# Performance work log

Hardware: AMD Instinct MI355X
Metric: run time of the kernel (lower is better)

The kernel has to match this reference:

```python
import jax, jax.numpy as jnp
import numpy as np
from jax import lax

B, W, M = 4, 20, 512
RNN_HID = 64
N_HIDDEN = RNN_HID          # bi = False
HALF = N_HIDDEN // 2
K = 10
LONG_K = W // 2             # conv_long kernel
LONG_OUT = W - 2 * (LONG_K - 1)   # = 2
N_SPATIAL = 10


def setup_inputs() -> dict:
    key = jax.random.key(0)
    ks = jax.random.split(key, 24)
    g = lambda i, shape, s=0.05: jax.random.normal(ks[i], shape, jnp.float32) * s
    return {
        "x": jax.random.normal(ks[0], (B, W, M), jnp.float32),
        # vanilla RNN (tanh), 1 layer, input_size=1
        "W_ih": g(1, (RNN_HID, 1), 0.2), "W_hh": g(2, (RNN_HID, RNN_HID), 0.1),
        "b_ih": g(3, (RNN_HID,)), "b_hh": g(4, (RNN_HID,)),
        # attention adjacency params
        "W1": g(5, (HALF, N_HIDDEN), 0.1), "b1": g(6, (HALF,)),
        "W2": g(7, (HALF, N_HIDDEN), 0.1),
        "V": g(8, (HALF,), 0.1), "bv": g(9, (1,)),
        "Wb": g(10, (M, M), 0.05), "wb": g(11, (1,)),
        # conv / conv_long
        "conv_w": g(12, (K, 1, W), 0.1), "conv_b": g(13, (K,)),
        "convl_w": g(14, (K, 1, LONG_K), 0.1), "convl_b": g(15, (K,)),
        # graph conv layers: adj @ (x @ W) + b
        "gc1_w": g(16, ((1 + LONG_OUT) * K, N_HIDDEN), 0.1), "gc1_b": g(17, (N_HIDDEN,)),
        "gc2_w": g(18, (N_HIDDEN, N_SPATIAL), 0.1), "gc2_b": g(19, (N_SPATIAL,)),
        # output head
        "out_w": g(20, (1, N_HIDDEN + N_SPATIAL), 0.1), "out_b": g(21, (1,)),
        # fixed geographic adjacency (data.adj)
        "adj": jax.random.uniform(ks[22], (M, M), dtype=jnp.float32),
    }


def _conv1d(x, w, b, dilation=1):
    # x: (N, Cin, W), w: (Cout, Cin, K) -> (N, Cout, Wout), VALID padding
    y = lax.conv_general_dilated(x, w, (1,), 'VALID', rhs_dilation=(dilation,),
                                 dimension_numbers=('NCH', 'OIH', 'NCH'))
    return y + b[None, :, None]


def reference(x, W_ih, W_hh, b_ih, b_hh, W1, b1, W2, V, bv, Wb, wb,
              conv_w, conv_b, convl_w, convl_b, gc1_w, gc1_b, gc2_w, gc2_b,
              out_w, out_b, adj):
    b, w, m = x.shape
    # ---- RNN encode each node's scalar series: (b*m, w, 1) -> last hidden ----
    xr = jnp.transpose(x, (0, 2, 1)).reshape(b * m, w)          # (bm, w)
    inp = xr[..., None] @ W_ih.T + b_ih                         # (bm, w, H)

    def step(h, u):
        return jnp.tanh(u + h @ W_hh.T + b_hh), None

    h0 = jnp.zeros((b * m, RNN_HID), x.dtype)
    h_last, _ = lax.scan(step, h0, jnp.swapaxes(inp, 0, 1))     # (bm, H)
    last_hid = h_last.reshape(b, m, N_HIDDEN)
    out_temporal = last_hid

    # ---- pairwise bilinear attention adjacency (broadcast instead of repeat) ----
    p = last_hid @ W1.T                                         # (b, m, H/2)
    q = last_hid @ W2.T                                         # (b, m, H/2)
    e = jax.nn.elu(p[:, :, None, :] + q[:, None, :, :] + b1)    # (b, m, m, H/2)
    a_mx = e @ V + bv[0]                                        # (b, m, m)
    # F.normalize(p=2, dim=1)
    nrm = jnp.maximum(jnp.sqrt(jnp.sum(a_mx * a_mx, axis=1, keepdims=True)), 1e-12)
    a_mx = a_mx / nrm
    c = jax.nn.sigmoid(a_mx @ Wb + wb[0])                       # (b, m, m)
    A = adj[None] * c + a_mx * (1.0 - c)

    # ---- per-node convs, batched over all b*m series (no Python loop) ----
    h_tmp = xr[:, None, :]                                      # (bm, 1, w)
    r = _conv1d(h_tmp, conv_w, conv_b)                          # (bm, k, 1)
    r_long = _conv1d(h_tmp, convl_w, convl_b, dilation=2)       # (bm, k, long_out)
    r_l = jnp.concatenate([r, r_long], axis=-1).reshape(b, m, -1)  # (b, m, (1+lo)*k)
    r_l = jax.nn.relu(r_l)

    # ---- graph convolutions: adj @ (x @ W) + b ----
    xg = jax.nn.relu(A @ (r_l @ gc1_w) + gc1_b)                 # (b, m, H)
    out_spatial = jax.nn.relu(A @ (xg @ gc2_w) + gc2_b)         # (b, m, 10)

    out = jnp.concatenate([out_spatial, out_temporal], axis=-1)
    return (out @ out_w.T + out_b)[..., 0]                      # (b, m)
```

## Files before the change

### kernel.cpp

```cpp
#include <hip/hip_runtime.h>
#include <hip/hip_bf16.h>
#include <cstdint>
#include <cstddef>

#define OFF_P     0
#define OFF_QB    65536
#define OFF_TDOT  131072
#define OFF_COLSQ 133120
#define OFF_ZT    135168
#define OFF_AMXB  155648
#define OFF_ABF   679936
#define OFF_G1T   1204224
#define OFF_WBT   1269760

typedef __attribute__((ext_vector_type(8))) short short8;
typedef __attribute__((ext_vector_type(8))) unsigned short ushort8;
typedef __attribute__((ext_vector_type(4))) float f32x4;

__device__ inline unsigned short f2bf(float f) {
    unsigned u = __builtin_bit_cast(unsigned, f);
    unsigned r = u + 0x7FFFu + ((u >> 16) & 1u);
    return (unsigned short)(r >> 16);
}
__device__ inline unsigned short f2bf_fast(float f) {
    unsigned u = __builtin_bit_cast(unsigned, f);
    return (unsigned short)((u + 0x8000u) >> 16);
}
__device__ inline float bf2f(unsigned short s) {
    unsigned u = ((unsigned)s) << 16;
    return __builtin_bit_cast(float, u);
}
__device__ inline float tanh_fast(float x) {
    return 1.f - 2.f/(__expf(2.f*x) + 1.f);
}

__global__ __launch_bounds__(256) void k1_rnn(
    const float* __restrict__ x, const float* __restrict__ W_ih,
    const float* __restrict__ W_hh, const float* __restrict__ b_ih,
    const float* __restrict__ b_hh, const float* __restrict__ W1,
    const float* __restrict__ b1, const float* __restrict__ W2,
    const float* __restrict__ conv_w, const float* __restrict__ conv_b,
    const float* __restrict__ convl_w, const float* __restrict__ convl_b,
    const float* __restrict__ gc1_w, const float* __restrict__ out_w,
    const float* __restrict__ out_b, const float* __restrict__ Wb,
    float* __restrict__ p_out, float* __restrict__ qb_out,
    unsigned short* __restrict__ G1T, float* __restrict__ tdot,
    float* __restrict__ colsq, unsigned short* __restrict__ WbT)
{
    __shared__ float h_sh[4][64];
    __shared__ float xt_sh[4][20];
    __shared__ float rl_sh[4][30];
    __shared__ float tile[64][68];
    int tid = threadIdx.x;

    if (blockIdx.x >= 512) {
        int tt = blockIdx.x - 512;
        int k0 = (tt >> 3) * 64, j0 = (tt & 7) * 64;
        #pragma unroll
        for (int q = 0; q < 4; ++q) {
            int kr = (tid>>4) + 16*q;
            int jc = (tid&15)*4;
            *(float4*)&tile[kr][jc] = *(const float4*)(Wb + (size_t)(k0+kr)*512 + j0 + jc);
        }
        __syncthreads();
        int jl = tid>>2, kc = (tid&3)*16;
        int j = j0 + jl;
        ushort8 v0, v1;
        #pragma unroll
        for (int kk = 0; kk < 8; ++kk) v0[kk] = f2bf(tile[kc+kk][jl]);
        #pragma unroll
        for (int kk = 0; kk < 8; ++kk) v1[kk] = f2bf(tile[kc+8+kk][jl]);
        unsigned short* dst = WbT + (size_t)j*512 + k0 + kc;
        *(ushort8*)dst = v0;
        *(ushort8*)(dst+8) = v1;
        return;
    }

    int w = tid >> 6, lane = tid & 63;
    int s = blockIdx.x * 4 + w;
    int b = s >> 9, m = s & 511;

    if (blockIdx.x < 8) colsq[blockIdx.x * 256 + tid] = 0.f;

    if (lane < 20) xt_sh[w][lane] = x[(b*20 + lane)*512 + m];

    float wrow[64];
    const float* wr = W_hh + lane*64;
    #pragma unroll
    for (int k4 = 0; k4 < 16; ++k4) {
        float4 v = reinterpret_cast<const float4*>(wr)[k4];
        wrow[4*k4+0]=v.x; wrow[4*k4+1]=v.y; wrow[4*k4+2]=v.z; wrow[4*k4+3]=v.w;
    }
    float wih = W_ih[lane], bih = b_ih[lane], bhh = b_hh[lane];
    h_sh[w][lane] = 0.f;
    float h = 0.f;

    if (lane < 10) {
        float acc = conv_b[lane];
        #pragma unroll
        for (int t = 0; t < 20; ++t) acc += conv_w[lane*20+t]*xt_sh[w][t];
        rl_sh[w][3*lane] = fmaxf(acc, 0.f);
    } else if (lane < 30) {
        int idx = lane-10, j = idx>>1, oo = idx&1;
        float acc = convl_b[j];
        #pragma unroll
        for (int t = 0; t < 10; ++t) acc += convl_w[j*10+t]*xt_sh[w][oo+2*t];
        rl_sh[w][3*j+1+oo] = fmaxf(acc, 0.f);
    }

    for (int t = 0; t < 20; ++t) {
        float a0=0.f, a1=0.f, a2=0.f, a3=0.f;
        #pragma unroll
        for (int k = 0; k < 64; k += 4) {
            a0 += wrow[k+0]*h_sh[w][k+0];
            a1 += wrow[k+1]*h_sh[w][k+1];
            a2 += wrow[k+2]*h_sh[w][k+2];
            a3 += wrow[k+3]*h_sh[w][k+3];
        }
        float acc = xt_sh[w][t]*wih + bih + bhh + ((a0+a1)+(a2+a3));
        h = tanh_fast(acc);
        h_sh[w][lane] = h;
    }

    float td = h * out_w[10 + lane];
    #pragma unroll
    for (int off = 32; off; off >>= 1) td += __shfl_down(td, off);
    if (lane == 0) tdot[s] = td + out_b[0];

    if (lane < 32) {
        const float* w1r = W1 + lane*64;
        float acc = 0.f;
        #pragma unroll
        for (int k = 0; k < 64; ++k) acc += w1r[k]*h_sh[w][k];
        p_out[s*32 + lane] = acc;
    } else {
        int i = lane - 32;
        const float* w2r = W2 + i*64;
        float acc = 0.f;
        #pragma unroll
        for (int k = 0; k < 64; ++k) acc += w2r[k]*h_sh[w][k];
        qb_out[s*32 + i] = acc + b1[i];
    }

    float g = 0.f;
    #pragma unroll
    for (int t = 0; t < 30; ++t) g += rl_sh[w][t]*gc1_w[t*64 + lane];
    G1T[((size_t)(b*64 + lane))*512 + m] = f2bf(g);
}

__global__ __launch_bounds__(256) void k2_amx(
    const float* __restrict__ p, const float* __restrict__ qb,
    const float* __restrict__ V, const float* __restrict__ bv,
    unsigned short* __restrict__ amxB, float* __restrict__ colsq)
{
    __shared__ float p_sh[32*36], q_sh[32*36], v_sh[32], sq_sh[32*17];
    int t = threadIdx.x;
    int b = blockIdx.z, i0 = blockIdx.y*32, j0 = blockIdx.x*32;
    {
        int r = t >> 3, c4 = (t & 7)*4;
        *(float4*)&p_sh[r*36 + c4] = *(const float4*)(p  + (size_t)(b*512 + i0 + r)*32 + c4);
        *(float4*)&q_sh[r*36 + c4] = *(const float4*)(qb + (size_t)(b*512 + j0 + r)*32 + c4);
    }
    if (t < 32) v_sh[t] = V[t];
    __syncthreads();

    int ti = t >> 4, tj = t & 15;
    float bv0 = bv[0];
    float a00 = bv0, a01 = bv0, a10 = bv0, a11 = bv0;
    #pragma unroll
    for (int h = 0; h < 32; ++h) {
        float p0 = p_sh[ti*36 + h], p1 = p_sh[(ti+16)*36 + h];
        float q0 = q_sh[tj*36 + h], q1 = q_sh[(tj+16)*36 + h];
        float vh = v_sh[h];
        float x00 = p0+q0, x01 = p0+q1, x10 = p1+q0, x11 = p1+q1;
        float e00 = x00 > 0.f ? x00 : __expf(x00)-1.f;
        float e01 = x01 > 0.f ? x01 : __expf(x01)-1.f;
        float e10 = x10 > 0.f ? x10 : __expf(x10)-1.f;
        float e11 = x11 > 0.f ? x11 : __expf(x11)-1.f;
        a00 += vh*e00; a01 += vh*e01; a10 += vh*e10; a11 += vh*e11;
    }
    size_t base0 = ((size_t)(b*512 + i0 + ti))*512 + j0;
    size_t base1 = ((size_t)(b*512 + i0 + ti + 16))*512 + j0;
    amxB[base0 + tj]      = f2bf(a00);
    amxB[base0 + tj + 16] = f2bf(a01);
    amxB[base1 + tj]      = f2bf(a10);
    amxB[base1 + tj + 16] = f2bf(a11);

    sq_sh[tj*17 + ti]      = a00*a00 + a10*a10;
    sq_sh[(tj+16)*17 + ti] = a01*a01 + a11*a11;
    __syncthreads();
    if (t < 32) {
        float ssum = 0.f;
        #pragma unroll
        for (int r = 0; r < 16; ++r) ssum += sq_sh[t*17 + r];
        atomicAdd(&colsq[b*512 + j0 + t], ssum);
    }
}

__global__ __launch_bounds__(256) void k3a_mfma(
    const unsigned short* __restrict__ amxB, const unsigned short* __restrict__ WbT,
    const float* __restrict__ colsq, const float* __restrict__ wb,
    const float* __restrict__ adj, unsigned short* __restrict__ Abf)
{
    __shared__ unsigned short amx_save[4][32*40];
    int tid = threadIdx.x;
    int wv = tid >> 6, lane = tid & 63;
    int b = blockIdx.z;
    int i0 = blockIdx.y*32;
    int j0 = blockIdx.x*128 + wv*32;

    f32x4 acc[2][2] = {};

    int sl = (lane>>4)*8;
    int fr = lane & 15;
    const unsigned short* abase = amxB + ((size_t)(b*512 + i0 + fr))*512 + sl;
    const unsigned short* bbase = WbT  + ((size_t)(j0 + fr))*512 + sl;
    const float* csq = colsq + b*512 + sl;

    #pragma unroll 2
    for (int k0 = 0; k0 < 512; k0 += 32) {
        float4 c0 = *(const float4*)(csq + k0);
        float4 c1 = *(const float4*)(csq + k0 + 4);
        float iv[8] = {
            rsqrtf(fmaxf(c0.x,1e-24f)), rsqrtf(fmaxf(c0.y,1e-24f)),
            rsqrtf(fmaxf(c0.z,1e-24f)), rsqrtf(fmaxf(c0.w,1e-24f)),
            rsqrtf(fmaxf(c1.x,1e-24f)), rsqrtf(fmaxf(c1.y,1e-24f)),
            rsqrtf(fmaxf(c1.z,1e-24f)), rsqrtf(fmaxf(c1.w,1e-24f)) };

        short8 a0r = *(const short8*)(abase + k0);
        short8 a1r = *(const short8*)(abase + 16*512 + k0);
        short8 b0  = *(const short8*)(bbase + k0);
        short8 b1  = *(const short8*)(bbase + 16*512 + k0);

        if (k0 == j0) {
            *(short8*)&amx_save[wv][fr*40 + sl]      = a0r;
            *(short8*)&amx_save[wv][(fr+16)*40 + sl] = a1r;
        }

        short8 a0, a1;
        #pragma unroll
        for (int e = 0; e < 8; ++e) {
            a0[e] = (short)f2bf_fast(bf2f((unsigned short)a0r[e]) * iv[e]);
            a1[e] = (short)f2bf_fast(bf2f((unsigned short)a1r[e]) * iv[e]);
        }

        acc[0][0] = __builtin_amdgcn_mfma_f32_16x16x32_bf16(a0, b0, acc[0][0],0,0,0);
        acc[0][1] = __builtin_amdgcn_mfma_f32_16x16x32_bf16(a0, b1, acc[0][1],0,0,0);
        acc[1][0] = __builtin_amdgcn_mfma_f32_16x16x32_bf16(a1, b0, acc[1][0],0,0,0);
        acc[1][1] = __builtin_amdgcn_mfma_f32_16x16x32_bf16(a1, b1, acc[1][1],0,0,0);
    }

    float wbs = wb[0];
    #pragma unroll
    for (int fj = 0; fj < 2; ++fj) {
        int j = j0 + fj*16 + fr;
        float inv = rsqrtf(fmaxf(colsq[b*512 + j], 1e-24f));
        #pragma unroll
        for (int fi = 0; fi < 2; ++fi)
        #pragma unroll
        for (int r = 0; r < 4; ++r) {
            int il = fi*16 + (lane>>4)*4 + r;
            int i = i0 + il;
            float S = acc[fi][fj][r] + wbs;
            float c = 1.f/(1.f + __expf(-S));
            float aN = bf2f(amx_save[wv][il*40 + fj*16 + fr]) * inv;
            Abf[((size_t)(b*512)+i)*512 + j] = f2bf(adj[(size_t)i*512+j]*c + aN*(1.f - c));
        }
    }
}

#define AS_STRIDE 520
__global__ __launch_bounds__(256) void k3b_mfma(
    const unsigned short* __restrict__ Abf, const unsigned short* __restrict__ G1T,
    const float* __restrict__ gc1_b, const float* __restrict__ gc2_w,
    float* __restrict__ zT)
{
    __shared__ __align__(16) unsigned short As[16*AS_STRIDE];
    __shared__ float xg[16][68];
    int t = threadIdx.x;
    int b = blockIdx.y, i0 = blockIdx.x*16;
    int wv = t >> 6, lane = t & 63;

    {
        int r = t >> 4, seg = (t & 15)*32;
        const unsigned short* src = Abf + ((size_t)(b*512 + i0 + r))*512 + seg;
        *(short8*)&As[r*AS_STRIDE + seg]      = *(const short8*)src;
        *(short8*)&As[r*AS_STRIDE + seg + 8]  = *(const short8*)(src + 8);
        *(short8*)&As[r*AS_STRIDE + seg + 16] = *(const short8*)(src + 16);
        *(short8*)&As[r*AS_STRIDE + seg + 24] = *(const short8*)(src + 24);
    }
    __syncthreads();

    f32x4 acc = {};
    const unsigned short* gbase = G1T + ((size_t)(b*64 + wv*16 + (lane&15)))*512 + (lane>>4)*8;
    int aoff = (lane&15)*AS_STRIDE + (lane>>4)*8;
    #pragma unroll 4
    for (int k0 = 0; k0 < 512; k0 += 32) {
        short8 af = *(const short8*)&As[aoff + k0];
        short8 bf = *(const short8*)(gbase + k0);
        acc = __builtin_amdgcn_mfma_f32_16x16x32_bf16(af, bf, acc, 0,0,0);
    }

    {
        int cc = wv*16 + (lane&15);
        float gb = gc1_b[cc];
        #pragma unroll
        for (int r = 0; r < 4; ++r)
            xg[(lane>>4)*4 + r][cc] = fmaxf(acc[r] + gb, 0.f);
    }
    __syncthreads();

    if (t < 160) {
        int row = t/10, sx = t%10;
        float a = 0.f;
        #pragma unroll
        for (int c = 0; c < 64; ++c) a += xg[row][c]*gc2_w[c*10 + sx];
        zT[((size_t)(b*10) + sx)*512 + i0 + row] = a;
    }
}

__global__ __launch_bounds__(256) void k4_out(
    const unsigned short* __restrict__ Abf, const float* __restrict__ zT,
    const float* __restrict__ gc2_b, const float* __restrict__ out_w,
    const float* __restrict__ tdot, float* __restrict__ out)
{
    int t = threadIdx.x;
    int w = t >> 6, lane = t & 63;

    #pragma unroll
    for (int rep = 0; rep < 2; ++rep) {
        int s = blockIdx.x*8 + w*2 + rep;
        int b = s >> 9;

        short8 av = *(const short8*)(Abf + (size_t)s*512 + lane*8);
        float a[8];
        #pragma unroll
        for (int q = 0; q < 8; ++q) a[q] = bf2f((unsigned short)av[q]);

        float acc[10];
        #pragma unroll
        for (int sx = 0; sx < 10; ++sx) {
            const float* zr = zT + ((size_t)(b*10) + sx)*512 + lane*8;
            float4 z0 = *(const float4*)zr;
            float4 z1 = *(const float4*)(zr + 4);
            acc[sx] = a[0]*z0.x + a[1]*z0.y + a[2]*z0.z + a[3]*z0.w
                    + a[4]*z1.x + a[5]*z1.y + a[6]*z1.z + a[7]*z1.w;
        }
        #pragma unroll
        for (int sx = 0; sx < 10; ++sx)
            #pragma unroll
            for (int off = 32; off; off >>= 1) acc[sx] += __shfl_down(acc[sx], off);
        if (lane == 0) {
            float o = tdot[s];
            #pragma unroll
            for (int sx = 0; sx < 10; ++sx)
                o += fmaxf(acc[sx] + gc2_b[sx], 0.f) * out_w[sx];
            out[s] = o;
        }
    }
}

extern "C" void kernel_launch(void* const* d_in, const int* in_sizes, int n_in,
                              void* d_out, int out_size, void* d_ws, size_t ws_size,
                              hipStream_t stream) {
    const float* x       = (const float*)d_in[0];
    const float* W_ih    = (const float*)d_in[1];
    const float* W_hh    = (const float*)d_in[2];
    const float* b_ih    = (const float*)d_in[3];
    const float* b_hh    = (const float*)d_in[4];
    const float* W1      = (const float*)d_in[5];
    const float* b1      = (const float*)d_in[6];
    const float* W2      = (const float*)d_in[7];
    const float* V       = (const float*)d_in[8];
    const float* bv      = (const float*)d_in[9];
    const float* Wb      = (const float*)d_in[10];
    const float* wb      = (const float*)d_in[11];
    const float* conv_w  = (const float*)d_in[12];
    const float* conv_b  = (const float*)d_in[13];
    const float* convl_w = (const float*)d_in[14];
    const float* convl_b = (const float*)d_in[15];
    const float* gc1_w   = (const float*)d_in[16];
    const float* gc1_b   = (const float*)d_in[17];
    const float* gc2_w   = (const float*)d_in[18];
    const float* gc2_b   = (const float*)d_in[19];
    const float* out_w   = (const float*)d_in[20];
    const float* out_b   = (const float*)d_in[21];
    const float* adj     = (const float*)d_in[22];

    float* ws    = (float*)d_ws;
    float* p     = ws + OFF_P;
    float* qb    = ws + OFF_QB;
    float* tdot  = ws + OFF_TDOT;
    float* colsq = ws + OFF_COLSQ;
    float* zT    = ws + OFF_ZT;
    unsigned short* amxB = (unsigned short*)(ws + OFF_AMXB);
    unsigned short* Abf  = (unsigned short*)(ws + OFF_ABF);
    unsigned short* G1T  = (unsigned short*)(ws + OFF_G1T);
    unsigned short* WbT  = (unsigned short*)(ws + OFF_WBT);
    float* out   = (float*)d_out;

    k1_rnn<<<dim3(576), dim3(256), 0, stream>>>(
        x, W_ih, W_hh, b_ih, b_hh, W1, b1, W2,
        conv_w, conv_b, convl_w, convl_b, gc1_w, out_w, out_b, Wb,
        p, qb, G1T, tdot, colsq, WbT);

    k2_amx<<<dim3(16,16,4), dim3(256), 0, stream>>>(p, qb, V, bv, amxB, colsq);

    k3a_mfma<<<dim3(4,16,4), dim3(256), 0, stream>>>(amxB, WbT, colsq, wb, adj, Abf);

    k3b_mfma<<<dim3(32,4), dim3(256), 0, stream>>>(Abf, G1T, gc1_b, gc2_w, zT);

    k4_out<<<dim3(256), dim3(256), 0, stream>>>(Abf, zT, gc2_b, out_w, tdot, out);
}
```

Measured before the change: 61.00 us.

## Fuse first graph-conv matmul into A-building kernel via atomic partial sums

Each k3 tile now also multiplies its freshly computed A block by the matching G1T slice and atomically accumulates partial xg pre-activations into a zeroed fp32 buffer. The buffer is cleared inside k2. The separate k3b kernel is removed, and k4 now recomputes relu(xg+b)@gc2_w per block into shared memory before the second aggregation. This saves a launch and a re-read of A, at the cost of many float atomics and every k4 block redundantly recomputing z for its whole batch.

```diff
diff --git a/kernel.cpp b/kernel.cpp
--- a/kernel.cpp
+++ b/kernel.cpp
@@ -7,11 +7,11 @@
 #define OFF_QB    65536
 #define OFF_TDOT  131072
 #define OFF_COLSQ 133120
-#define OFF_ZT    135168
-#define OFF_AMXB  155648
-#define OFF_ABF   679936
-#define OFF_G1T   1204224
-#define OFF_WBT   1269760
+#define OFF_XGP   135168
+#define OFF_AMXB  266240
+#define OFF_ABF   790528
+#define OFF_G1T   1314816
+#define OFF_WBT   1380352
 
 typedef __attribute__((ext_vector_type(8))) short short8;
 typedef __attribute__((ext_vector_type(8))) unsigned short ushort8;
@@ -151,11 +151,19 @@
 __global__ __launch_bounds__(256) void k2_amx(
     const float* __restrict__ p, const float* __restrict__ qb,
     const float* __restrict__ V, const float* __restrict__ bv,
-    unsigned short* __restrict__ amxB, float* __restrict__ colsq)
+    unsigned short* __restrict__ amxB, float* __restrict__ colsq,
+    float* __restrict__ xg_pre)
 {
     __shared__ float p_sh[32*36], q_sh[32*36], v_sh[32], sq_sh[32*17];
     int t = threadIdx.x;
     int b = blockIdx.z, i0 = blockIdx.y*32, j0 = blockIdx.x*32;
+
+    int fb = (blockIdx.z<<8) | (blockIdx.y<<4) | blockIdx.x;
+    if (fb < 128) {
+        float4 zz = {0.f,0.f,0.f,0.f};
+        *(float4*)&xg_pre[(size_t)fb*1024 + t*4] = zz;
+    }
+
     {
         int r = t >> 3, c4 = (t & 7)*4;
         *(float4*)&p_sh[r*36 + c4] = *(const float4*)(p  + (size_t)(b*512 + i0 + r)*32 + c4);
@@ -197,12 +205,14 @@
     }
 }
 
-__global__ __launch_bounds__(256) void k3a_mfma(
+__global__ __launch_bounds__(256) void k3_mfma(
     const unsigned short* __restrict__ amxB, const unsigned short* __restrict__ WbT,
-    const float* __restrict__ colsq, const float* __restrict__ wb,
-    const float* __restrict__ adj, unsigned short* __restrict__ Abf)
+    const unsigned short* __restrict__ G1T, const float* __restrict__ colsq,
+    const float* __restrict__ wb, const float* __restrict__ adj,
+    unsigned short* __restrict__ Abf, float* __restrict__ xg_pre)
 {
     __shared__ unsigned short amx_save[4][32*40];
+    __shared__ unsigned short Atr[4][32*40];
     int tid = threadIdx.x;
     int wv = tid >> 6, lane = tid & 63;
     int b = blockIdx.z;
@@ -253,98 +263,107 @@
     float wbs = wb[0];
     #pragma unroll
     for (int fj = 0; fj < 2; ++fj) {
-        int j = j0 + fj*16 + fr;
+        int jl = fj*16 + fr;
+        int j = j0 + jl;
         float inv = rsqrtf(fmaxf(colsq[b*512 + j], 1e-24f));
         #pragma unroll
         for (int fi = 0; fi < 2; ++fi)
         #pragma unroll
         for (int r = 0; r < 4; ++r) {
             int il = fi*16 + (lane>>4)*4 + r;
-            int i = i0 + il;
             float S = acc[fi][fj][r] + wbs;
             float c = 1.f/(1.f + __expf(-S));
-            float aN = bf2f(amx_save[wv][il*40 + fj*16 + fr]) * inv;
-            Abf[((size_t)(b*512)+i)*512 + j] = f2bf(adj[(size_t)i*512+j]*c + aN*(1.f - c));
-        }
-    }
-}
-
-#define AS_STRIDE 520
-__global__ __launch_bounds__(256) void k3b_mfma(
-    const unsigned short* __restrict__ Abf, const unsigned short* __restrict__ G1T,
+            float aN = bf2f(amx_save[wv][il*40 + jl]) * inv;
+            unsigned short u = f2bf(adj[(size_t)(i0+il)*512 + j]*c + aN*(1.f - c));
+            Abf[((size_t)(b*512) + i0 + il)*512 + j] = u;
+            Atr[wv][il*40 + jl] = u;
+        }
+    }
+
+    short8 aT0 = *(const short8*)&Atr[wv][fr*40 + sl];
+    short8 aT1 = *(const short8*)&Atr[wv][(fr+16)*40 + sl];
+    f32x4 acc2[2][4] = {};
+    #pragma unroll
+    for (int cb = 0; cb < 4; ++cb) {
+        short8 gfrag = *(const short8*)(G1T + ((size_t)(b*64 + cb*16 + fr))*512 + j0 + sl);
+        acc2[0][cb] = __builtin_amdgcn_mfma_f32_16x16x32_bf16(aT0, gfrag, acc2[0][cb],0,0,0);
+        acc2[1][cb] = __builtin_amdgcn_mfma_f32_16x16x32_bf16(aT1, gfrag, acc2[1][cb],0,0,0);
+    }
+    #pragma unroll
+    for (int fi = 0; fi < 2; ++fi)
+    #pragma unroll
+    for (int cb = 0; cb < 4; ++cb)
+    #pragma unroll
+    for (int rr = 0; rr < 4; ++rr) {
+        int i = i0 + fi*16 + (lane>>4)*4 + rr;
+        int c = cb*16 + fr;
+        atomicAdd(&xg_pre[((size_t)(b*512) + i)*64 + c], acc2[fi][cb][rr]);
+    }
+}
+
+__global__ __launch_bounds__(256) void k4_out(
+    const unsigned short* __restrict__ Abf, const float* __restrict__ xg_pre,
     const float* __restrict__ gc1_b, const float* __restrict__ gc2_w,
-    float* __restrict__ zT)
-{
-    __shared__ __align__(16) unsigned short As[16*AS_STRIDE];
-    __shared__ float xg[16][68];
-    int t = threadIdx.x;
-    int b = blockIdx.y, i0 = blockIdx.x*16;
-    int wv = t >> 6, lane = t & 63;
-
-    {
-        int r = t >> 4, seg = (t & 15)*32;
-        const unsigned short* src = Abf + ((size_t)(b*512 + i0 + r))*512 + seg;
-        *(short8*)&As[r*AS_STRIDE + seg]      = *(const short8*)src;
-        *(short8*)&As[r*AS_STRIDE + seg + 8]  = *(const short8*)(src + 8);
-        *(short8*)&As[r*AS_STRIDE + seg + 16] = *(const short8*)(src + 16);
-        *(short8*)&As[r*AS_STRIDE + seg + 24] = *(const short8*)(src + 24);
-    }
-    __syncthreads();
-
-    f32x4 acc = {};
-    const unsigned short* gbase = G1T + ((size_t)(b*64 + wv*16 + (lane&15)))*512 + (lane>>4)*8;
-    int aoff = (lane&15)*AS_STRIDE + (lane>>4)*8;
-    #pragma unroll 4
-    for (int k0 = 0; k0 < 512; k0 += 32) {
-        short8 af = *(const short8*)&As[aoff + k0];
-        short8 bf = *(const short8*)(gbase + k0);
-        acc = __builtin_amdgcn_mfma_f32_16x16x32_bf16(af, bf, acc, 0,0,0);
-    }
-
-    {
-        int cc = wv*16 + (lane&15);
-        float gb = gc1_b[cc];
-        #pragma unroll
-        for (int r = 0; r < 4; ++r)
-            xg[(lane>>4)*4 + r][cc] = fmaxf(acc[r] + gb, 0.f);
-    }
-    __syncthreads();
-
-    if (t < 160) {
-        int row = t/10, sx = t%10;
-        float a = 0.f;
-        #pragma unroll
-        for (int c = 0; c < 64; ++c) a += xg[row][c]*gc2_w[c*10 + sx];
-        zT[((size_t)(b*10) + sx)*512 + i0 + row] = a;
-    }
-}
-
-__global__ __launch_bounds__(256) void k4_out(
-    const unsigned short* __restrict__ Abf, const float* __restrict__ zT,
     const float* __restrict__ gc2_b, const float* __restrict__ out_w,
     const float* __restrict__ tdot, float* __restrict__ out)
 {
+    __shared__ float z_l[10*512];
+    __shared__ float g2w[640];
+    __shared__ float g1b[64];
     int t = threadIdx.x;
+    int bid = blockIdx.x;
+    int b = bid >> 6;
+    int i0 = (bid & 63) * 8;
+
+    for (int idx = t; idx < 640; idx += 256) g2w[idx] = gc2_w[idx];
+    if (t < 64) g1b[t] = gc1_b[t];
+    __syncthreads();
+
+    {
+        const float* xr0 = xg_pre + ((size_t)(b*512) + t)*64;
+        const float* xr1 = xr0 + 256*64;
+        float acc0[10] = {}, acc1[10] = {};
+        #pragma unroll 4
+        for (int c = 0; c < 64; c += 4) {
+            float4 va = *(const float4*)(xr0 + c);
+            float4 vb = *(const float4*)(xr1 + c);
+            float aa[4] = {va.x,va.y,va.z,va.w};
+            float bb[4] = {vb.x,vb.y,vb.z,vb.w};
+            #pragma unroll
+            for (int e = 0; e < 4; ++e) {
+                float v0 = fmaxf(aa[e] + g1b[c+e], 0.f);
+                float v1 = fmaxf(bb[e] + g1b[c+e], 0.f);
+                #pragma unroll
+                for (int sx = 0; sx < 10; ++sx) {
+                    float wgt = g2w[(c+e)*10 + sx];
+                    acc0[sx] += v0*wgt;
+                    acc1[sx] += v1*wgt;
+                }
+            }
+        }
+        #pragma unroll
+        for (int sx = 0; sx < 10; ++sx) {
+            z_l[sx*512 + t]       = acc0[sx];
+            z_l[sx*512 + t + 256] = acc1[sx];
+        }
+    }
+    __syncthreads();
+
     int w = t >> 6, lane = t & 63;
-
     #pragma unroll
     for (int rep = 0; rep < 2; ++rep) {
-        int s = blockIdx.x*8 + w*2 + rep;
-        int b = s >> 9;
-
-        short8 av = *(const short8*)(Abf + (size_t)s*512 + lane*8);
+        int s = b*512 + i0 + w*2 + rep;
         float a[8];
         #pragma unroll
-        for (int q = 0; q < 8; ++q) a[q] = bf2f((unsigned short)av[q]);
-
+        for (int q = 0; q < 8; ++q)
+            a[q] = bf2f(Abf[(size_t)s*512 + q*64 + lane]);
         float acc[10];
         #pragma unroll
         for (int sx = 0; sx < 10; ++sx) {
-            const float* zr = zT + ((size_t)(b*10) + sx)*512 + lane*8;
-            float4 z0 = *(const float4*)zr;
-            float4 z1 = *(const float4*)(zr + 4);
-            acc[sx] = a[0]*z0.x + a[1]*z0.y + a[2]*z0.z + a[3]*z0.w
-                    + a[4]*z1.x + a[5]*z1.y + a[6]*z1.z + a[7]*z1.w;
+            float ssum = 0.f;
+            #pragma unroll
+            for (int q = 0; q < 8; ++q) ssum += a[q]*z_l[sx*512 + q*64 + lane];
+            acc[sx] = ssum;
         }
         #pragma unroll
         for (int sx = 0; sx < 10; ++sx)
@@ -392,7 +411,7 @@
     float* qb    = ws + OFF_QB;
     float* tdot  = ws + OFF_TDOT;
     float* colsq = ws + OFF_COLSQ;
-    float* zT    = ws + OFF_ZT;
+    float* xg_pre = ws + OFF_XGP;
     unsigned short* amxB = (unsigned short*)(ws + OFF_AMXB);
     unsigned short* Abf  = (unsigned short*)(ws + OFF_ABF);
     unsigned short* G1T  = (unsigned short*)(ws + OFF_G1T);
@@ -404,11 +423,11 @@
         conv_w, conv_b, convl_w, convl_b, gc1_w, out_w, out_b, Wb,
         p, qb, G1T, tdot, colsq, WbT);
 
-    k2_amx<<<dim3(16,16,4), dim3(256), 0, stream>>>(p, qb, V, bv, amxB, colsq);
-
-    k3a_mfma<<<dim3(4,16,4), dim3(256), 0, stream>>>(amxB, WbT, colsq, wb, adj, Abf);
-
-    k3b_mfma<<<dim3(32,4), dim3(256), 0, stream>>>(Abf, G1T, gc1_b, gc2_w, zT);
-
-    k4_out<<<dim3(256), dim3(256), 0, stream>>>(Abf, zT, gc2_b, out_w, tdot, out);
-}
+    k2_amx<<<dim3(16,16,4), dim3(256), 0, stream>>>(p, qb, V, bv, amxB, colsq, xg_pre);
+
+    k3_mfma<<<dim3(4,16,4), dim3(256), 0, stream>>>(
+        amxB, WbT, G1T, colsq, wb, adj, Abf, xg_pre);
+
+    k4_out<<<dim3(256), dim3(256), 0, stream>>>(
+        Abf, xg_pre, gc1_b, gc2_w, gc2_b, out_w, tdot, out);
+}
```

Result: slower. 68.90 us (+12.9%).
